# Optimization experiments

Hardware: AMD Instinct MI355X
Metric: run time of the kernel (lower is better)

## Reference

```python
import jax, jax.numpy as jnp
import numpy as np

N, I, O = 256, 1024, 1024

def setup_inputs() -> dict:
    key = jax.random.key(0)
    k1, k2, k3, k4 = jax.random.split(key, 4)
    x = jax.random.normal(k1, (N, I), dtype=jnp.float32)
    # attention acts as a soft drop-connect mask in [0, 1)
    attention = jax.random.uniform(k2, (N, I, O), dtype=jnp.float32)
    # kaiming-ish init scale for a linear layer
    weight = jax.random.normal(k3, (O, I), dtype=jnp.float32) * (1.0 / np.sqrt(I))
    bias_param = jax.random.normal(k4, (O,), dtype=jnp.float32) * 0.01
    return {"x": x, "attention": attention, "weight": weight, "bias_param": bias_param}

def reference(x, attention, weight, bias_param):
    # Per-sample attention-modulated linear:
    # out[n, o] = sum_i x[n, i] * weight[o, i] * attention[n, i, o] + bias[o]
    # Single fused contraction; never materializes the [N, O, I] modulated weight.
    out = jnp.einsum('ni,oi,nio->no', x, weight, attention)
    return out + bias_param
```

## Files before the change

kernel.cpp:

```cpp
#include <hip/hip_runtime.h>


typedef float f32x4 __attribute__((ext_vector_type(4)));

constexpr int Nn = 256;
constexpr int Ii = 1024;
constexpr int Oo = 1024;
constexpr int ISPLIT = 8;
constexpr int IRANGE = Ii / ISPLIT;
constexpr int NB = 4;
constexpr int TPB = 256;

__global__ __launch_bounds__(256)
void transpose_w_kernel(const float* __restrict__ w, float* __restrict__ wT) {
    __shared__ float tile[32][33];
    const int bi = blockIdx.x * 32;
    const int bo = blockIdx.y * 32;
    const int tx = threadIdx.x % 32;
    const int ty = threadIdx.x / 32;
    #pragma unroll
    for (int r = 0; r < 4; ++r)
        tile[ty + 8 * r][tx] = w[(size_t)(bo + ty + 8 * r) * Ii + bi + tx];
    __syncthreads();
    #pragma unroll
    for (int r = 0; r < 4; ++r)
        wT[(size_t)(bi + ty + 8 * r) * Oo + bo + tx] = tile[tx][ty + 8 * r];
}

__global__ __launch_bounds__(TPB)
void attn_partial_kernel(const float* __restrict__ x,
                         const float* __restrict__ att,
                         const float* __restrict__ wT,
                         float* __restrict__ partial) {
    __shared__ float xs4[IRANGE][NB];

    const int s   = blockIdx.x;
    const int ng  = blockIdx.y;
    const int tid = threadIdx.x;
    const int i0  = s * IRANGE;
    const int n0  = ng * NB;

    if (tid < IRANGE) {
        #pragma unroll
        for (int j = 0; j < NB; ++j)
            xs4[tid][j] = x[(size_t)(n0 + j) * Ii + i0 + tid];
    }
    __syncthreads();

    const int o0 = tid * 4;
    const float* a0p = att + ((size_t)(n0 + 0) * Ii + i0) * Oo + o0;
    const float* a1p = att + ((size_t)(n0 + 1) * Ii + i0) * Oo + o0;
    const float* a2p = att + ((size_t)(n0 + 2) * Ii + i0) * Oo + o0;
    const float* a3p = att + ((size_t)(n0 + 3) * Ii + i0) * Oo + o0;
    const float* wtp = wT + (size_t)i0 * Oo + o0;

    f32x4 acc0 = {0.f, 0.f, 0.f, 0.f};
    f32x4 acc1 = {0.f, 0.f, 0.f, 0.f};
    f32x4 acc2 = {0.f, 0.f, 0.f, 0.f};
    f32x4 acc3 = {0.f, 0.f, 0.f, 0.f};

#define ROW(ii)                                                              \
    {                                                                        \
        const size_t roff = (size_t)(ii) * Oo;                               \
        f32x4 wv = *reinterpret_cast<const f32x4*>(wtp + roff);              \
        f32x4 xv = *reinterpret_cast<const f32x4*>(&xs4[ii][0]);             \
        f32x4 b0 = __builtin_nontemporal_load(                               \
            reinterpret_cast<const f32x4*>(a0p + roff));                     \
        f32x4 b1 = __builtin_nontemporal_load(                               \
            reinterpret_cast<const f32x4*>(a1p + roff));                     \
        f32x4 b2 = __builtin_nontemporal_load(                               \
            reinterpret_cast<const f32x4*>(a2p + roff));                     \
        f32x4 b3 = __builtin_nontemporal_load(                               \
            reinterpret_cast<const f32x4*>(a3p + roff));                     \
        _Pragma("unroll")                                                    \
        for (int k = 0; k < 4; ++k) {                                        \
            acc0[k] = fmaf(xv[0] * wv[k], b0[k], acc0[k]);                   \
            acc1[k] = fmaf(xv[1] * wv[k], b1[k], acc1[k]);                   \
            acc2[k] = fmaf(xv[2] * wv[k], b2[k], acc2[k]);                   \
            acc3[k] = fmaf(xv[3] * wv[k], b3[k], acc3[k]);                   \
        }                                                                    \
    }

    #pragma unroll 2
    for (int i = 0; i < IRANGE; i += 2) {
        ROW(i + 0)
        ROW(i + 1)
    }
#undef ROW

    float* pp = partial + ((size_t)s * Nn + n0) * Oo + o0;
    *reinterpret_cast<f32x4*>(pp + 0 * (size_t)Oo) = acc0;
    *reinterpret_cast<f32x4*>(pp + 1 * (size_t)Oo) = acc1;
    *reinterpret_cast<f32x4*>(pp + 2 * (size_t)Oo) = acc2;
    *reinterpret_cast<f32x4*>(pp + 3 * (size_t)Oo) = acc3;
}

__global__ __launch_bounds__(TPB)
void attn_reduce_kernel(const float* __restrict__ partial,
                        const float* __restrict__ bias,
                        float* __restrict__ out) {
    const int n   = blockIdx.x;
    const int tid = threadIdx.x;
    const int o0  = tid * 4;

    f32x4 acc = *reinterpret_cast<const f32x4*>(bias + o0);
    #pragma unroll
    for (int s = 0; s < ISPLIT; ++s) {
        f32x4 p = *reinterpret_cast<const f32x4*>(
            partial + ((size_t)s * Nn + n) * Oo + o0);
        acc[0] += p[0]; acc[1] += p[1]; acc[2] += p[2]; acc[3] += p[3];
    }
    *reinterpret_cast<f32x4*>(out + (size_t)n * Oo + o0) = acc;
}

extern "C" void kernel_launch(void* const* d_in, const int* in_sizes, int n_in,
                              void* d_out, int out_size, void* d_ws, size_t ws_size,
                              hipStream_t stream) {
    const float* x    = (const float*)d_in[0];
    const float* att  = (const float*)d_in[1];
    const float* w    = (const float*)d_in[2];
    const float* bias = (const float*)d_in[3];
    float* out        = (float*)d_out;

    float* partial = (float*)d_ws;
    float* wT      = (float*)((char*)d_ws + (size_t)ISPLIT * Nn * Oo * sizeof(float));

    dim3 tgrid(Ii / 32, Oo / 32);
    transpose_w_kernel<<<tgrid, 256, 0, stream>>>(w, wT);

    dim3 grid1(ISPLIT, Nn / NB);
    attn_partial_kernel<<<grid1, TPB, 0, stream>>>(x, att, wT, partial);

    attn_reduce_kernel<<<Nn, TPB, 0, stream>>>(partial, bias, out);
}
```

Measured before the change: 191.5 us.

## Fuse split-I partial sums and reduction into one kernel via LDS

Replaces the two-pass split-I scheme (partial buffer in global memory plus a separate reduce kernel) with a single kernel. Each block covers a 128-wide output chunk, and its 8 waves each take a slice of I; the partial sums are reduced in shared memory and bias is added there. This removes the global partial-sum traffic and one kernel launch. In exchange, each wave reads shorter contiguous runs of the attention tensor and the block uses more shared memory, which may lower occupancy.

Measured after the change: 182.5 us (median of 2 runs). 4.7% less time.

```diff
diff --git a/kernel.cpp b/kernel.cpp
--- a/kernel.cpp
+++ b/kernel.cpp
@@ -6,9 +6,10 @@
 constexpr int Nn = 256;
 constexpr int Ii = 1024;
 constexpr int Oo = 1024;
-constexpr int ISPLIT = 8;
-constexpr int IRANGE = Ii / ISPLIT;
 constexpr int NB = 4;
+constexpr int OCHUNK = 128;
+constexpr int NSUB = 8;
+constexpr int ISUB = Ii / NSUB;
 constexpr int TPB = 256;
 
 __global__ __launch_bounds__(256)
@@ -28,26 +29,31 @@
 }
 
 __global__ __launch_bounds__(TPB)
-void attn_partial_kernel(const float* __restrict__ x,
-                         const float* __restrict__ att,
-                         const float* __restrict__ wT,
-                         float* __restrict__ partial) {
-    __shared__ float xs4[IRANGE][NB];
+void attn_fused_kernel(const float* __restrict__ x,
+                       const float* __restrict__ att,
+                       const float* __restrict__ wT,
+                       const float* __restrict__ bias,
+                       float* __restrict__ out) {
+    __shared__ float xs[NB][Ii];
+    __shared__ float red[NSUB][NB * OCHUNK];
 
-    const int s   = blockIdx.x;
+    const int ocx = blockIdx.x;
     const int ng  = blockIdx.y;
     const int tid = threadIdx.x;
-    const int i0  = s * IRANGE;
+    const int g   = tid >> 5;
+    const int t   = tid & 31;
     const int n0  = ng * NB;
+    const int oc0 = ocx * OCHUNK;
 
-    if (tid < IRANGE) {
-        #pragma unroll
-        for (int j = 0; j < NB; ++j)
-            xs4[tid][j] = x[(size_t)(n0 + j) * Ii + i0 + tid];
-    }
+    #pragma unroll
+    for (int nb = 0; nb < NB; ++nb)
+        reinterpret_cast<f32x4*>(&xs[nb][0])[tid] =
+            reinterpret_cast<const f32x4*>(x + (size_t)(n0 + nb) * Ii)[tid];
     __syncthreads();
 
-    const int o0 = tid * 4;
+    const int i0 = g * ISUB;
+    const int o0 = oc0 + t * 4;
+
     const float* a0p = att + ((size_t)(n0 + 0) * Ii + i0) * Oo + o0;
     const float* a1p = att + ((size_t)(n0 + 1) * Ii + i0) * Oo + o0;
     const float* a2p = att + ((size_t)(n0 + 2) * Ii + i0) * Oo + o0;
@@ -59,58 +65,55 @@
     f32x4 acc2 = {0.f, 0.f, 0.f, 0.f};
     f32x4 acc3 = {0.f, 0.f, 0.f, 0.f};
 
-#define ROW(ii)                                                              \
-    {                                                                        \
-        const size_t roff = (size_t)(ii) * Oo;                               \
-        f32x4 wv = *reinterpret_cast<const f32x4*>(wtp + roff);              \
-        f32x4 xv = *reinterpret_cast<const f32x4*>(&xs4[ii][0]);             \
-        f32x4 b0 = __builtin_nontemporal_load(                               \
-            reinterpret_cast<const f32x4*>(a0p + roff));                     \
-        f32x4 b1 = __builtin_nontemporal_load(                               \
-            reinterpret_cast<const f32x4*>(a1p + roff));                     \
-        f32x4 b2 = __builtin_nontemporal_load(                               \
-            reinterpret_cast<const f32x4*>(a2p + roff));                     \
-        f32x4 b3 = __builtin_nontemporal_load(                               \
-            reinterpret_cast<const f32x4*>(a3p + roff));                     \
-        _Pragma("unroll")                                                    \
-        for (int k = 0; k < 4; ++k) {                                        \
-            acc0[k] = fmaf(xv[0] * wv[k], b0[k], acc0[k]);                   \
-            acc1[k] = fmaf(xv[1] * wv[k], b1[k], acc1[k]);                   \
-            acc2[k] = fmaf(xv[2] * wv[k], b2[k], acc2[k]);                   \
-            acc3[k] = fmaf(xv[3] * wv[k], b3[k], acc3[k]);                   \
-        }                                                                    \
+    for (int ii = 0; ii < ISUB; ii += 4) {
+        f32x4 xv0 = *reinterpret_cast<const f32x4*>(&xs[0][i0 + ii]);
+        f32x4 xv1 = *reinterpret_cast<const f32x4*>(&xs[1][i0 + ii]);
+        f32x4 xv2 = *reinterpret_cast<const f32x4*>(&xs[2][i0 + ii]);
+        f32x4 xv3 = *reinterpret_cast<const f32x4*>(&xs[3][i0 + ii]);
+        #pragma unroll
+        for (int e = 0; e < 4; ++e) {
+            const size_t roff = (size_t)(ii + e) * Oo;
+            f32x4 wv = *reinterpret_cast<const f32x4*>(wtp + roff);
+            f32x4 b0 = __builtin_nontemporal_load(
+                reinterpret_cast<const f32x4*>(a0p + roff));
+            f32x4 b1 = __builtin_nontemporal_load(
+                reinterpret_cast<const f32x4*>(a1p + roff));
+            f32x4 b2 = __builtin_nontemporal_load(
+                reinterpret_cast<const f32x4*>(a2p + roff));
+            f32x4 b3 = __builtin_nontemporal_load(
+                reinterpret_cast<const f32x4*>(a3p + roff));
+            #pragma unroll
+            for (int k = 0; k < 4; ++k) {
+                acc0[k] = fmaf(xv0[e] * wv[k], b0[k], acc0[k]);
+                acc1[k] = fmaf(xv1[e] * wv[k], b1[k], acc1[k]);
+                acc2[k] = fmaf(xv2[e] * wv[k], b2[k], acc2[k]);
+                acc3[k] = fmaf(xv3[e] * wv[k], b3[k], acc3[k]);
+            }
+        }
     }
 
-    #pragma unroll 2
-    for (int i = 0; i < IRANGE; i += 2) {
-        ROW(i + 0)
-        ROW(i + 1)
+    *reinterpret_cast<f32x4*>(&red[g][0 * OCHUNK + t * 4]) = acc0;
+    *reinterpret_cast<f32x4*>(&red[g][1 * OCHUNK + t * 4]) = acc1;
+    *reinterpret_cast<f32x4*>(&red[g][2 * OCHUNK + t * 4]) = acc2;
+    *reinterpret_cast<f32x4*>(&red[g][3 * OCHUNK + t * 4]) = acc3;
+    __syncthreads();
+
+    {
+        const int fl = tid * 2;
+        const int nb = fl >> 7;
+        const int ol = fl & 127;
+        float sx = 0.f, sy = 0.f;
+        #pragma unroll
+        for (int g2 = 0; g2 < NSUB; ++g2) {
+            const float* rp = &red[g2][fl];
+            sx += rp[0];
+            sy += rp[1];
+        }
+        sx += bias[oc0 + ol];
+        sy += bias[oc0 + ol + 1];
+        float2 res = {sx, sy};
+        *reinterpret_cast<float2*>(out + (size_t)(n0 + nb) * Oo + oc0 + ol) = res;
     }
-#undef ROW
-
-    float* pp = partial + ((size_t)s * Nn + n0) * Oo + o0;
-    *reinterpret_cast<f32x4*>(pp + 0 * (size_t)Oo) = acc0;
-    *reinterpret_cast<f32x4*>(pp + 1 * (size_t)Oo) = acc1;
-    *reinterpret_cast<f32x4*>(pp + 2 * (size_t)Oo) = acc2;
-    *reinterpret_cast<f32x4*>(pp + 3 * (size_t)Oo) = acc3;
-}
-
-__global__ __launch_bounds__(TPB)
-void attn_reduce_kernel(const float* __restrict__ partial,
-                        const float* __restrict__ bias,
-                        float* __restrict__ out) {
-    const int n   = blockIdx.x;
-    const int tid = threadIdx.x;
-    const int o0  = tid * 4;
-
-    f32x4 acc = *reinterpret_cast<const f32x4*>(bias + o0);
-    #pragma unroll
-    for (int s = 0; s < ISPLIT; ++s) {
-        f32x4 p = *reinterpret_cast<const f32x4*>(
-            partial + ((size_t)s * Nn + n) * Oo + o0);
-        acc[0] += p[0]; acc[1] += p[1]; acc[2] += p[2]; acc[3] += p[3];
-    }
-    *reinterpret_cast<f32x4*>(out + (size_t)n * Oo + o0) = acc;
 }
 
 extern "C" void kernel_launch(void* const* d_in, const int* in_sizes, int n_in,
@@ -121,15 +124,11 @@
     const float* w    = (const float*)d_in[2];
     const float* bias = (const float*)d_in[3];
     float* out        = (float*)d_out;
-
-    float* partial = (float*)d_ws;
-    float* wT      = (float*)((char*)d_ws + (size_t)ISPLIT * Nn * Oo * sizeof(float));
+    float* wT         = (float*)d_ws;
 
     dim3 tgrid(Ii / 32, Oo / 32);
     transpose_w_kernel<<<tgrid, 256, 0, stream>>>(w, wT);
 
-    dim3 grid1(ISPLIT, Nn / NB);
-    attn_partial_kernel<<<grid1, TPB, 0, stream>>>(x, att, wT, partial);
-
-    attn_reduce_kernel<<<Nn, TPB, 0, stream>>>(partial, bias, out);
+    dim3 grid(Oo / OCHUNK, Nn / NB);
+    attn_fused_kernel<<<grid, TPB, 0, stream>>>(x, att, wT, bias, out);
 }
```
